# Optimization experiments

Hardware: AMD Instinct MI355X
Metric: run time of the kernel (lower is better)

The kernel has to match this reference:

```python
import jax, jax.numpy as jnp
import numpy as np


def setup_inputs() -> dict:
    key = jax.random.key(0)
    k = jax.random.split(key, 6)
    B, H, W, C = 16, 128, 128, 256
    NH, KD, VD = 8, 64, 64
    return {
        "key_value": jax.random.normal(k[0], (B, H, W, C), dtype=jnp.float32),
        "Wk": jax.random.normal(k[1], (C, NH * KD), dtype=jnp.float32) * (C ** -0.5),
        "bk": jnp.zeros((NH * KD,), dtype=jnp.float32),
        "Wv": jax.random.normal(k[2], (C, NH * VD), dtype=jnp.float32) * (C ** -0.5),
        "bv": jnp.zeros((NH * VD,), dtype=jnp.float32),
        "query": jax.random.normal(k[3], (1, 1, NH, KD), dtype=jnp.float32) * 0.05,
    }


def reference(key_value, Wk, bk, Wv, bv, query):
    B, H, W, C = key_value.shape
    _, _, NH, KD = query.shape
    VD = Wv.shape[1] // NH
    S = H * W  # flattened spatial length
    kv = key_value.reshape(B, S, C)
    # 1x1 conv == per-pixel dense projection
    k = (kv @ Wk + bk).reshape(B, S, NH, KD)   # [B,S,NH,KD]
    v = (kv @ Wv + bv).reshape(B, S, NH, VD)   # [B,S,NH,VD]
    # learned query dotted with keys (no sqrt scaling in original)
    scores = jnp.einsum("bshd,hd->bsh", k, query[0, 0])  # [B,S,NH]
    probs = jax.nn.softmax(scores, axis=1)                 # softmax over spatial axis
    out = jnp.einsum("bsh,bshd->bhd", probs, v)            # [B,NH,VD]
    return out
```

## Files before the change

### kernel.cpp

```cpp
#include <hip/hip_runtime.h>
#include <stdint.h>

typedef unsigned short u16;
typedef unsigned int u32;

typedef __attribute__((ext_vector_type(8))) __bf16 bf16x8;
typedef __attribute__((ext_vector_type(4))) float f32x4;

#define SDIM 16384
#define CDIM 256

__device__ __forceinline__ u16 f2bf(float f) {
    union { float f; u32 i; } v; v.f = f;
    u32 r = v.i + 0x7FFFu + ((v.i >> 16) & 1u);
    return (u16)(r >> 16);
}
__device__ __forceinline__ float bf_lo(u32 w) { union { u32 i; float f; } v; v.i = w << 16;        return v.f; }
__device__ __forceinline__ float bf_hi(u32 w) { union { u32 i; float f; } v; v.i = w & 0xFFFF0000u; return v.f; }

__global__ __launch_bounds__(256) void k_prep(const float* __restrict__ Wk,
                                              const float* __restrict__ bk,
                                              const float* __restrict__ q,
                                              u16* __restrict__ wqb_g,
                                              float* __restrict__ bq) {
    int idx = blockIdx.x * 256 + threadIdx.x;
    int h = idx >> 8, c = idx & 255;
    float s = 0.f;
    if (h < 8) {
        const float4* wp = (const float4*)(Wk + (size_t)c * 512 + h * 64);
        const float4* qp = (const float4*)(q + h * 64);
        #pragma unroll
        for (int j = 0; j < 16; ++j) {
            float4 w = wp[j], qq = qp[j];
            s += w.x * qq.x + w.y * qq.y + w.z * qq.z + w.w * qq.w;
        }
    }
    wqb_g[h * 256 + c] = f2bf(s);
    if (idx < 8) {
        float sb = 0.f;
        for (int d = 0; d < 64; ++d) sb += bk[idx * 64 + d] * q[idx * 64 + d];
        bq[idx] = sb;
    }
}

__global__ __launch_bounds__(256, 3) void k_main(const float* __restrict__ kv,
                                                 const u16* __restrict__ wqb_g,
                                                 const float* __restrict__ bq_g,
                                                 float* __restrict__ partials,
                                                 float* __restrict__ zpart) {
    __shared__ u16 klds[64 * 264];
    __shared__ u16 wqb[16 * 264];
    __shared__ float pl[64 * 8];
    __shared__ float zp[4 * 8];

    const int t = threadIdx.x;
    const int lane = t & 63;
    const int wave = t >> 6;
    const int blk = blockIdx.x;
    const int b = blk >> 6, grp = blk & 63;

    {
        int i0 = t, i1 = t + 256;
        int h0 = i0 >> 5, k0 = i0 & 31;
        int h1 = i1 >> 5, k1 = i1 & 31;
        *(uint4*)&wqb[h0 * 264 + k0 * 8] = *(const uint4*)&wqb_g[h0 * 256 + k0 * 8];
        *(uint4*)&wqb[h1 * 264 + k1 * 8] = *(const uint4*)&wqb_g[h1 * 256 + k1 * 8];
    }
    __syncthreads();

    const int h16 = lane & 15, q4 = lane >> 4;
    bf16x8 bfrag[8];
    #pragma unroll
    for (int ks = 0; ks < 8; ++ks) {
        uint4 r = *(const uint4*)&wqb[h16 * 264 + ks * 32 + q4 * 8];
        bfrag[ks] = __builtin_bit_cast(bf16x8, r);
    }
    const float bqv = (h16 < 8) ? bq_g[h16] : 0.f;
    const int px0 = wave * 16;
    const int sg = t & 3, cg = t >> 2;

    float tac[32];
    #pragma unroll
    for (int i = 0; i < 32; ++i) tac[i] = 0.f;
    float zacc = 0.f;

    const size_t pixbase = (size_t)(b << 14) + grp * 256;

    for (int it = 0; it < 4; ++it) {
        const float4* kvp = (const float4*)(kv + (pixbase + it * 64) * CDIM);
        #pragma unroll
        for (int j = 0; j < 16; ++j) {
            int f = j * 256 + t;
            float4 g = kvp[f];
            uint2 w;
            w.x = (u32)f2bf(g.x) | ((u32)f2bf(g.y) << 16);
            w.y = (u32)f2bf(g.z) | ((u32)f2bf(g.w) << 16);
            *(uint2*)&klds[(f >> 6) * 264 + (f & 63) * 4] = w;
        }
        __syncthreads();

        f32x4 acc = {0.f, 0.f, 0.f, 0.f};
        #pragma unroll
        for (int ks = 0; ks < 8; ++ks) {
            uint4 r = *(const uint4*)&klds[(px0 + h16) * 264 + ks * 32 + q4 * 8];
            bf16x8 a = __builtin_bit_cast(bf16x8, r);
            acc = __builtin_amdgcn_mfma_f32_16x16x32_bf16(a, bfrag[ks], acc, 0, 0, 0);
        }
        float e0 = __expf(acc[0] + bqv);
        float e1 = __expf(acc[1] + bqv);
        float e2 = __expf(acc[2] + bqv);
        float e3 = __expf(acc[3] + bqv);
        if (h16 < 8) {
            pl[(px0 + q4 * 4 + 0) * 8 + h16] = e0;
            pl[(px0 + q4 * 4 + 1) * 8 + h16] = e1;
            pl[(px0 + q4 * 4 + 2) * 8 + h16] = e2;
            pl[(px0 + q4 * 4 + 3) * 8 + h16] = e3;
        }
        float zv = e0 + e1 + e2 + e3;
        zv += __shfl_xor(zv, 16);
        zv += __shfl_xor(zv, 32);
        zacc += zv;
        __syncthreads();

        #pragma unroll 4
        for (int i = 0; i < 16; ++i) {
            int px = sg + i * 4;
            uint2 kw = *(const uint2*)&klds[px * 264 + cg * 4];
            float k0 = bf_lo(kw.x), k1 = bf_hi(kw.x);
            float k2 = bf_lo(kw.y), k3 = bf_hi(kw.y);
            float4 p0 = *(const float4*)&pl[px * 8];
            float4 p1 = *(const float4*)&pl[px * 8 + 4];
            float ph[8] = {p0.x, p0.y, p0.z, p0.w, p1.x, p1.y, p1.z, p1.w};
            #pragma unroll
            for (int h = 0; h < 8; ++h) {
                tac[h * 4 + 0] += k0 * ph[h];
                tac[h * 4 + 1] += k1 * ph[h];
                tac[h * 4 + 2] += k2 * ph[h];
                tac[h * 4 + 3] += k3 * ph[h];
            }
        }
        __syncthreads();
    }

    if (lane < 8) zp[wave * 8 + lane] = zacc;
    __syncthreads();
    if (t < 8) zpart[blk * 8 + t] = zp[t] + zp[8 + t] + zp[16 + t] + zp[24 + t];

    #pragma unroll
    for (int i = 0; i < 32; ++i) {
        tac[i] += __shfl_xor(tac[i], 1);
        tac[i] += __shfl_xor(tac[i], 2);
    }
    if (sg == 0) {
        float* pb = partials + (size_t)blk * 2048;
        #pragma unroll
        for (int h = 0; h < 8; ++h) {
            float4 v = {tac[h * 4 + 0], tac[h * 4 + 1], tac[h * 4 + 2], tac[h * 4 + 3]};
            *(float4*)&pb[h * 256 + cg * 4] = v;
        }
    }
}

__global__ __launch_bounds__(256) void k_out(const float* __restrict__ partials,
                                             const float* __restrict__ zpart,
                                             const float* __restrict__ Wv,
                                             const float* __restrict__ bv,
                                             float* __restrict__ out) {
    __shared__ float tlds[256];
    __shared__ float zsh;
    int bh = blockIdx.x;
    int b = bh >> 3, h = bh & 7, t = threadIdx.x;

    const float* p = partials + (size_t)(b * 64) * 2048 + h * 256 + t;
    float s = 0.f;
    #pragma unroll 8
    for (int j = 0; j < 64; ++j) s += p[(size_t)j * 2048];
    tlds[t] = s;

    if (t < 64) {
        float zv = zpart[(b * 64 + t) * 8 + h];
        #pragma unroll
        for (int o = 32; o > 0; o >>= 1) zv += __shfl_xor(zv, o);
        if (t == 0) zsh = zv;
    }
    __syncthreads();

    if (t < 64) {
        int d = t;
        const float* wv = Wv + h * 64 + d;
        float acc = 0.f;
        #pragma unroll 8
        for (int c = 0; c < 256; ++c)
            acc += tlds[c] * wv[(size_t)c * 512];
        out[bh * 64 + d] = acc / zsh + bv[h * 64 + d];
    }
}

extern "C" void kernel_launch(void* const* d_in, const int* in_sizes, int n_in,
                              void* d_out, int out_size, void* d_ws, size_t ws_size,
                              hipStream_t stream) {
    const float* kv = (const float*)d_in[0];
    const float* Wk = (const float*)d_in[1];
    const float* bk = (const float*)d_in[2];
    const float* Wv = (const float*)d_in[3];
    const float* bv = (const float*)d_in[4];
    const float* q  = (const float*)d_in[5];

    char* ws = (char*)d_ws;
    u16*   wqb_g    = (u16*)(ws);
    float* bq       = (float*)(ws + 8192);
    float* partials = (float*)(ws + 16384);
    float* zpart    = (float*)(ws + 16384 + 8388608);

    k_prep<<<16,   256, 0, stream>>>(Wk, bk, q, wqb_g, bq);
    k_main<<<1024, 256, 0, stream>>>(kv, wqb_g, bq, partials, zpart);
    k_out <<<128,  256, 0, stream>>>(partials, zpart, Wv, bv, (float*)d_out);
}
```

Baseline: 395.4 us.

## Load key_value tiles directly into LDS as fp32 with XOR swizzle

Replaces the register-staged global load plus bf16 conversion with global_load_lds DMA that writes fp32 tiles straight into shared memory, using an XOR swizzle on the 16-byte chunk index to avoid bank conflicts. The bf16 packing moves to the MFMA operand read, and the weighted-sum pass now uses fp32 keys from LDS. This doubles the LDS tile size, so occupancy hint drops from 3 to 2 blocks, and the loads are still not overlapped with compute across iterations.

```diff
diff --git a/kernel.cpp b/kernel.cpp
--- a/kernel.cpp
+++ b/kernel.cpp
@@ -9,14 +9,20 @@
 
 #define SDIM 16384
 #define CDIM 256
+
+#define GLD_LDS16(g, l)                                                        \
+    __builtin_amdgcn_global_load_lds(                                          \
+        (__attribute__((address_space(1))) const void*)(g),                    \
+        (__attribute__((address_space(3))) void*)(l), 16, 0, 0)
 
 __device__ __forceinline__ u16 f2bf(float f) {
     union { float f; u32 i; } v; v.f = f;
     u32 r = v.i + 0x7FFFu + ((v.i >> 16) & 1u);
     return (u16)(r >> 16);
 }
-__device__ __forceinline__ float bf_lo(u32 w) { union { u32 i; float f; } v; v.i = w << 16;        return v.f; }
-__device__ __forceinline__ float bf_hi(u32 w) { union { u32 i; float f; } v; v.i = w & 0xFFFF0000u; return v.f; }
+__device__ __forceinline__ u32 pkbf(float a, float b) {
+    return (u32)f2bf(a) | ((u32)f2bf(b) << 16);
+}
 
 __global__ __launch_bounds__(256) void k_prep(const float* __restrict__ Wk,
                                               const float* __restrict__ bk,
@@ -43,12 +49,12 @@
     }
 }
 
-__global__ __launch_bounds__(256, 3) void k_main(const float* __restrict__ kv,
+__global__ __launch_bounds__(256, 2) void k_main(const float* __restrict__ kv,
                                                  const u16* __restrict__ wqb_g,
                                                  const float* __restrict__ bq_g,
                                                  float* __restrict__ partials,
                                                  float* __restrict__ zpart) {
-    __shared__ u16 klds[64 * 264];
+    __shared__ float klds[64 * 256];
     __shared__ u16 wqb[16 * 264];
     __shared__ float pl[64 * 8];
     __shared__ float zp[4 * 8];
@@ -77,7 +83,8 @@
     }
     const float bqv = (h16 < 8) ? bq_g[h16] : 0.f;
     const int px0 = wave * 16;
-    const int sg = t & 3, cg = t >> 2;
+    const int arow = px0 + h16;
+    const int sg = lane & 3, cg = t >> 2;
 
     float tac[32];
     #pragma unroll
@@ -87,24 +94,26 @@
     const size_t pixbase = (size_t)(b << 14) + grp * 256;
 
     for (int it = 0; it < 4; ++it) {
-        const float4* kvp = (const float4*)(kv + (pixbase + it * 64) * CDIM);
+        const float* tb = kv + (pixbase + it * 64) * CDIM;
         #pragma unroll
         for (int j = 0; j < 16; ++j) {
-            int f = j * 256 + t;
-            float4 g = kvp[f];
-            uint2 w;
-            w.x = (u32)f2bf(g.x) | ((u32)f2bf(g.y) << 16);
-            w.y = (u32)f2bf(g.z) | ((u32)f2bf(g.w) << 16);
-            *(uint2*)&klds[(f >> 6) * 264 + (f & 63) * 4] = w;
+            int px = wave * 16 + j;
+            const float* gp = tb + px * CDIM + ((lane ^ px) & 63) * 4;
+            GLD_LDS16(gp, &klds[px * 256]);
         }
         __syncthreads();
 
         f32x4 acc = {0.f, 0.f, 0.f, 0.f};
         #pragma unroll
         for (int ks = 0; ks < 8; ++ks) {
-            uint4 r = *(const uint4*)&klds[(px0 + h16) * 264 + ks * 32 + q4 * 8];
-            bf16x8 a = __builtin_bit_cast(bf16x8, r);
-            acc = __builtin_amdgcn_mfma_f32_16x16x32_bf16(a, bfrag[ks], acc, 0, 0, 0);
+            int c4 = ks * 8 + q4 * 2;
+            float4 fa = *(const float4*)&klds[arow * 256 + ((c4 ^ arow) & 63) * 4];
+            float4 fb = *(const float4*)&klds[arow * 256 + (((c4 + 1) ^ arow) & 63) * 4];
+            uint4 r;
+            r.x = pkbf(fa.x, fa.y); r.y = pkbf(fa.z, fa.w);
+            r.z = pkbf(fb.x, fb.y); r.w = pkbf(fb.z, fb.w);
+            acc = __builtin_amdgcn_mfma_f32_16x16x32_bf16(
+                      __builtin_bit_cast(bf16x8, r), bfrag[ks], acc, 0, 0, 0);
         }
         float e0 = __expf(acc[0] + bqv);
         float e1 = __expf(acc[1] + bqv);
@@ -125,18 +134,16 @@
         #pragma unroll 4
         for (int i = 0; i < 16; ++i) {
             int px = sg + i * 4;
-            uint2 kw = *(const uint2*)&klds[px * 264 + cg * 4];
-            float k0 = bf_lo(kw.x), k1 = bf_hi(kw.x);
-            float k2 = bf_lo(kw.y), k3 = bf_hi(kw.y);
+            float4 kw = *(const float4*)&klds[px * 256 + ((cg ^ px) & 63) * 4];
             float4 p0 = *(const float4*)&pl[px * 8];
             float4 p1 = *(const float4*)&pl[px * 8 + 4];
             float ph[8] = {p0.x, p0.y, p0.z, p0.w, p1.x, p1.y, p1.z, p1.w};
             #pragma unroll
             for (int h = 0; h < 8; ++h) {
-                tac[h * 4 + 0] += k0 * ph[h];
-                tac[h * 4 + 1] += k1 * ph[h];
-                tac[h * 4 + 2] += k2 * ph[h];
-                tac[h * 4 + 3] += k3 * ph[h];
+                tac[h * 4 + 0] += kw.x * ph[h];
+                tac[h * 4 + 1] += kw.y * ph[h];
+                tac[h * 4 + 2] += kw.z * ph[h];
+                tac[h * 4 + 3] += kw.w * ph[h];
             }
         }
         __syncthreads();
```

New measurement: 388.8 us. About the same (-1.7%).
